# Kernel tuning notes

Hardware: AMD Instinct MI355X
Metric: run time of the kernel (lower is better)

## Reference

```python
import jax, jax.numpy as jnp
import numpy as np

B, S, E, H = 2, 2048, 1024, 16
HD = E // H  # 64
NEG = -1e24


def setup_inputs() -> dict:
    key = jax.random.key(0)
    ks = jax.random.split(key, 20)
    sc_e = 1.0 / np.sqrt(E)
    inp = {
        "q_matrix": jax.random.normal(ks[0], (B, S, E), jnp.float32),
        "k_matrix": jax.random.normal(ks[1], (B, S, E), jnp.float32),
        "v_matrix": jax.random.normal(ks[2], (B, S, E), jnp.float32),
        "mask": jax.random.randint(ks[3], (B, S, S), 0, 2).astype(bool),
        # global QKV projections (embed_dim -> embed_dim)
        "Wq": jax.random.normal(ks[4], (E, E), jnp.float32) * sc_e,
        "bq": jnp.zeros((E,), jnp.float32),
        "Wk": jax.random.normal(ks[5], (E, E), jnp.float32) * sc_e,
        "bk": jnp.zeros((E,), jnp.float32),
        "Wv": jax.random.normal(ks[6], (E, E), jnp.float32) * sc_e,
        "bv": jnp.zeros((E,), jnp.float32),
        # per-head QKV projections (embed_dim -> head_dim), batched over heads
        "Whq": jax.random.normal(ks[7], (H, E, HD), jnp.float32) * sc_e,
        "bhq": jnp.zeros((H, HD), jnp.float32),
        "Whk": jax.random.normal(ks[8], (H, E, HD), jnp.float32) * sc_e,
        "bhk": jnp.zeros((H, HD), jnp.float32),
        "Whv": jax.random.normal(ks[9], (H, E, HD), jnp.float32) * sc_e,
        "bhv": jnp.zeros((H, HD), jnp.float32),
        # output projection
        "Wo": jax.random.normal(ks[10], (E, E), jnp.float32) * sc_e,
        "bo": jnp.zeros((E,), jnp.float32),
    }
    return inp


def reference(q_matrix, k_matrix, v_matrix, mask, Wq, bq, Wk, bk, Wv, bv,
              Whq, bhq, Whk, bhk, Whv, bhv, Wo, bo):
    # global projections [B,S,E]
    qg = q_matrix @ Wq + bq
    kg = k_matrix @ Wk + bk
    vg = v_matrix @ Wv + bv
    # per-head projections -> [B,H,S,HD]
    qh = jnp.einsum('bse,hed->bhsd', qg, Whq) + bhq[None, :, None, :]
    kh = jnp.einsum('bse,hed->bhsd', kg, Whk) + bhk[None, :, None, :]
    vh = jnp.einsum('bse,hed->bhsd', vg, Whv) + bhv[None, :, None, :]
    # scaled dot-product attention, scores [B,H,S,S]
    scores = jnp.einsum('bhsd,bhtd->bhst', qh, kh) / jnp.sqrt(jnp.float32(HD))
    scores = jnp.where(mask[:, None, :, :], NEG, scores)
    weights = jax.nn.softmax(scores, axis=-1)
    out = jnp.einsum('bhst,bhtd->bhsd', weights, vh)
    # concat heads (head order along last dim, matching torch.cat)
    x = out.transpose(0, 2, 1, 3).reshape(out.shape[0], out.shape[2], E)
    return x @ Wo + bo
```

## Files before the change

### kernel.cpp

```cpp
#include <hip/hip_runtime.h>
#include <hip/hip_bf16.h>

typedef unsigned short us16;
typedef __attribute__((ext_vector_type(8))) short short8;
typedef __attribute__((ext_vector_type(4))) float float4v;

#define E_DIM 1024
#define S_LEN 2048
#define B_DIM 2
#define H_DIM 16
#define HD_DIM 64
#define M_ROWS 4096
#define SCALE2 0.18033688011112042f

__device__ __forceinline__ float b2f(us16 b) {
    return __uint_as_float(((unsigned int)b) << 16);
}
__device__ __forceinline__ us16 f2b(float f) {
    unsigned int u = __float_as_uint(f);
    unsigned int r = (u + 0x7fffu + ((u >> 16) & 1u)) >> 16;
    return (us16)r;
}

__device__ __forceinline__ void gload16(const us16* g, us16* lds_uniform_base) {
    __builtin_amdgcn_global_load_lds(
        (const __attribute__((address_space(1))) void*)g,
        (__attribute__((address_space(3))) void*)lds_uniform_base, 16, 0, 0);
}

__global__ __launch_bounds__(256) void prep(
    const float* __restrict__ q, const float* __restrict__ k, const float* __restrict__ v,
    const float* __restrict__ Wq, const float* __restrict__ Wk, const float* __restrict__ Wv,
    const float* __restrict__ Whq, const float* __restrict__ Whk, const float* __restrict__ Whv,
    const float* __restrict__ Wo,
    const float* __restrict__ bq, const float* __restrict__ bk, const float* __restrict__ bv,
    const float* __restrict__ bhq, const float* __restrict__ bhk, const float* __restrict__ bhv,
    const int* __restrict__ mask,
    us16* qb, us16* kb, us16* vb, us16* Wqb, us16* Wkb, us16* Wvb,
    us16* WhqT, us16* WhkT, us16* WhvT, us16* WoT,
    us16* marr,
    float* bcq, float* bck, float* bcv, float* zbias)
{
    __shared__ us16 tile[32][33];
    __shared__ float red[4][64];
    int blk = blockIdx.x, tid = threadIdx.x;

    if (blk < 7680) {
        const float* in; us16* out; int idx;
        if (blk < 6144) {
            int z = blk >> 11, rem = blk & 2047;
            in = z == 0 ? q : z == 1 ? k : v;
            out = z == 0 ? qb : z == 1 ? kb : vb;
            idx = (rem * 256 + tid) * 8;
        } else {
            int t = blk - 6144, z = t >> 9, rem = t & 511;
            in = z == 0 ? Wq : z == 1 ? Wk : Wv;
            out = z == 0 ? Wqb : z == 1 ? Wkb : Wvb;
            idx = (rem * 256 + tid) * 8;
        }
        float4 f0 = *(const float4*)(in + idx);
        float4 f1 = *(const float4*)(in + idx + 4);
        us16 t8[8] = {f2b(f0.x), f2b(f0.y), f2b(f0.z), f2b(f0.w),
                      f2b(f1.x), f2b(f1.y), f2b(f1.z), f2b(f1.w)};
        *(uint4*)(out + idx) = *(const uint4*)t8;
    } else if (blk < 11776) {
        int t = blk - 7680, z = t >> 10, rem = t & 1023;
        const float* in = z == 0 ? Whq : z == 1 ? Whk : z == 2 ? Whv : Wo;
        us16* out = z == 0 ? WhqT : z == 1 ? WhkT : z == 2 ? WhvT : WoT;
        int mode = (z < 3) ? 1 : 0;
        int bx = rem & 31, by = rem >> 5;
        int tx = tid & 31, ty = tid >> 5;
#pragma unroll
        for (int i = 0; i < 4; ++i) {
            int e = by * 32 + ty + i * 8;
            int c = bx * 32 + tx;
            size_t src;
            if (mode == 0) src = (size_t)e * E_DIM + c;
            else           src = ((size_t)(c >> 6) * E_DIM + e) * 64 + (c & 63);
            tile[ty + i * 8][tx] = f2b(in[src]);
        }
        __syncthreads();
#pragma unroll
        for (int i = 0; i < 4; ++i) {
            int c = bx * 32 + ty + i * 8;
            int e = by * 32 + tx;
            out[(size_t)c * E_DIM + e] = tile[tx][ty + i * 8];
        }
    } else if (blk < 15872) {
        int g = (blk - 11776) * 256 + tid;
        int lane = g & 63, ld = (g >> 6) & 1, wv = (g >> 7) & 7;
        int q0t = (g >> 10) & 15, ktz = (g >> 14) & 31, bb = g >> 19;
        int quad = lane >> 4, l16 = lane & 15;
        int qq = q0t * 128 + wv * 16 + l16;
        int t0 = ktz * 64 + ld * 32 + quad * 4;
        const int* mp = mask + ((size_t)bb * S_LEN + qq) * S_LEN + t0;
        int4 ma = *(const int4*)mp;
        int4 mb2 = *(const int4*)(mp + 16);
        const us16 NEGB = f2b(-1e38f);
        us16 t8[8];
        t8[0] = ma.x ? NEGB : (us16)0;  t8[1] = ma.y ? NEGB : (us16)0;
        t8[2] = ma.z ? NEGB : (us16)0;  t8[3] = ma.w ? NEGB : (us16)0;
        t8[4] = mb2.x ? NEGB : (us16)0; t8[5] = mb2.y ? NEGB : (us16)0;
        t8[6] = mb2.z ? NEGB : (us16)0; t8[7] = mb2.w ? NEGB : (us16)0;
        *(uint4*)&marr[(size_t)g * 8] = *(const uint4*)t8;
    } else if (blk < 15920) {
        int t = blk - 15872, z = t >> 4, h = t & 15;
        const float* bg = z == 0 ? bq : z == 1 ? bk : bv;
        const float* Wh = z == 0 ? Whq : z == 1 ? Whk : Whv;
        const float* bh = z == 0 ? bhq : z == 1 ? bhk : bhv;
        float* bc = z == 0 ? bcq : z == 1 ? bck : bcv;
        float sc = (z == 0) ? SCALE2 : 1.0f;
        int d = tid & 63, part = tid >> 6;
        float acc = 0.f;
        int j0 = part * 256;
        for (int j = j0; j < j0 + 256; ++j)
            acc += bg[j] * Wh[((size_t)h * E_DIM + j) * HD_DIM + d];
        red[part][d] = acc;
        __syncthreads();
        if (tid < 64)
            bc[h * 64 + tid] = (red[0][tid] + red[1][tid] + red[2][tid] + red[3][tid] + bh[h * 64 + tid]) * sc;
    } else {
        int i = (blk - 15920) * 256 + tid;
        if (i < 1024) zbias[i] = 0.f;
    }
}

#define BK 32

__device__ __forceinline__ void gemm_body(
    const us16* __restrict__ A, const us16* __restrict__ Bt,
    const float* __restrict__ bias, void* __restrict__ Cp,
    int M, int N, int K, int bxt, int byt, int omode)
{
    __shared__ us16 As[128 * BK];
    __shared__ us16 Bs[128 * BK];

    int tid = threadIdx.x;
    int wave = tid >> 6, lane = tid & 63;
    int quad = lane >> 4, l16 = lane & 15;
    int wm = (wave >> 1) * 64, wn = (wave & 1) * 64;
    int bm0 = byt * 128, bn0 = bxt * 128;
    int srow = lane >> 2;
    int gcol = (((lane & 3) ^ (srow & 3)) << 3);
    int rslot = ((quad ^ (l16 & 3)) << 3);

    float4v acc[4][4];
#pragma unroll
    for (int i = 0; i < 4; ++i)
#pragma unroll
        for (int j = 0; j < 4; ++j)
#pragma unroll
            for (int r = 0; r < 4; ++r) acc[i][j][r] = 0.f;

    for (int k0 = 0; k0 < K; k0 += BK) {
#pragma unroll
        for (int c = 0; c < 2; ++c) {
            int r0 = 32 * wave + 16 * c;
            gload16(A  + (size_t)(bm0 + r0 + srow) * K + k0 + gcol, &As[r0 * BK]);
            gload16(Bt + (size_t)(bn0 + r0 + srow) * K + k0 + gcol, &Bs[r0 * BK]);
        }
        __syncthreads();
        short8 af[4], bfr[4];
#pragma unroll
        for (int i = 0; i < 4; ++i)
            af[i] = *(const short8*)&As[(wm + i * 16 + l16) * BK + rslot];
#pragma unroll
        for (int j = 0; j < 4; ++j)
            bfr[j] = *(const short8*)&Bs[(wn + j * 16 + l16) * BK + rslot];
#pragma unroll
        for (int i = 0; i < 4; ++i)
#pragma unroll
            for (int j = 0; j < 4; ++j)
                acc[i][j] = __builtin_amdgcn_mfma_f32_16x16x32_bf16(af[i], bfr[j], acc[i][j], 0, 0, 0);
        __syncthreads();
    }

#pragma unroll
    for (int i = 0; i < 4; ++i) {
#pragma unroll
        for (int j = 0; j < 4; ++j) {
#pragma unroll
            for (int r = 0; r < 4; ++r) {
                int row = bm0 + wm + i * 16 + quad * 4 + r;
                int col = bn0 + wn + j * 16 + l16;
                float vv = acc[i][j][r] + ((omode == 3) ? bias[row] : bias[col]);
                if (omode == 1) {
                    int b = row >> 11, s = row & 2047, h = col >> 6, d = col & 63;
                    ((us16*)Cp)[(((size_t)(b * H_DIM + h) * S_LEN + s) * HD_DIM) + d] = f2b(vv);
                } else {
                    int h = row >> 6, d = row & 63, b = col >> 11, sl = col & 2047;
                    ((us16*)Cp)[(((size_t)(b * H_DIM + h) * HD_DIM + d) * S_LEN) + sl] = f2b(vv);
                }
            }
        }
    }
}

__global__ __launch_bounds__(256) void proj_all(
    const us16* __restrict__ qb, const us16* __restrict__ kb, const us16* __restrict__ vb,
    const us16* __restrict__ WcqT, const us16* __restrict__ WckT, const us16* __restrict__ WcvT,
    const float* __restrict__ bcq, const float* __restrict__ bck, const float* __restrict__ bcv,
    us16* __restrict__ qhb, us16* __restrict__ khb, us16* __restrict__ vtb)
{
    int bx = blockIdx.x;
    int z = bx >> 8, t = bx & 255;
    if (z == 0)      gemm_body(qb, WcqT, bcq, qhb, M_ROWS, E_DIM, E_DIM, t & 7, t >> 3, 1);
    else if (z == 1) gemm_body(kb, WckT, bck, khb, M_ROWS, E_DIM, E_DIM, t & 7, t >> 3, 1);
    else             gemm_body(WcvT, vb, bcv, vtb, E_DIM, M_ROWS, E_DIM, t & 31, t >> 5, 3);
}

template<int OMODE>
__device__ __forceinline__ void gemm64_body(
    const us16* __restrict__ A, const us16* __restrict__ Bt,
    const float* __restrict__ bias, void* __restrict__ Cp,
    int M, int N, int K, int bxt, int byt, float oscale)
{
    __shared__ us16 As[64 * BK];
    __shared__ us16 Bs[128 * BK];

    int tid = threadIdx.x;
    int wave = tid >> 6, lane = tid & 63;
    int quad = lane >> 4, l16 = lane & 15;
    int wm = (wave >> 1) * 32, wn = (wave & 1) * 64;
    int bm0 = byt * 64, bn0 = bxt * 128;
    int srow = lane >> 2;
    int gcol = (((lane & 3) ^ (srow & 3)) << 3);
    int rslot = ((quad ^ (l16 & 3)) << 3);

    float4v acc[2][4];
#pragma unroll
    for (int i = 0; i < 2; ++i)
#pragma unroll
        for (int j = 0; j < 4; ++j)
#pragma unroll
            for (int r = 0; r < 4; ++r) acc[i][j][r] = 0.f;

    for (int k0 = 0; k0 < K; k0 += BK) {
        gload16(A + (size_t)(bm0 + 16 * wave + srow) * K + k0 + gcol, &As[16 * wave * BK]);
#pragma unroll
        for (int c = 0; c < 2; ++c) {
            int r0 = 32 * wave + 16 * c;
            gload16(Bt + (size_t)(bn0 + r0 + srow) * K + k0 + gcol, &Bs[r0 * BK]);
        }
        __syncthreads();
        short8 af[2], bfr[4];
#pragma unroll
        for (int i = 0; i < 2; ++i)
            af[i] = *(const short8*)&As[(wm + i * 16 + l16) * BK + rslot];
#pragma unroll
        for (int j = 0; j < 4; ++j)
            bfr[j] = *(const short8*)&Bs[(wn + j * 16 + l16) * BK + rslot];
#pragma unroll
        for (int i = 0; i < 2; ++i)
#pragma unroll
            for (int j = 0; j < 4; ++j)
                acc[i][j] = __builtin_amdgcn_mfma_f32_16x16x32_bf16(af[i], bfr[j], acc[i][j], 0, 0, 0);
        __syncthreads();
    }

#pragma unroll
    for (int i = 0; i < 2; ++i)
#pragma unroll
        for (int j = 0; j < 4; ++j)
#pragma unroll
            for (int r = 0; r < 4; ++r) {
                int row = bm0 + wm + i * 16 + quad * 4 + r;
                int col = bn0 + wn + j * 16 + l16;
                float vv = (acc[i][j][r] + bias[col]) * oscale;
                if (OMODE == 0) ((us16*)Cp)[(size_t)row * N + col] = f2b(vv);
                else            ((float*)Cp)[(size_t)row * N + col] = vv;
            }
}

__global__ __launch_bounds__(256) void wgemm3(
    const us16* A0, const us16* A1, const us16* A2,
    const us16* B0, const us16* B1, const us16* B2,
    const float* zbias, us16* C0, us16* C1, us16* C2)
{
    int z = blockIdx.z;
    const us16* A = z == 0 ? A0 : z == 1 ? A1 : A2;
    const us16* Bt = z == 0 ? B0 : z == 1 ? B1 : B2;
    us16* C = z == 0 ? C0 : z == 1 ? C1 : C2;
    float sc = (z == 0) ? SCALE2 : 1.0f;
    gemm64_body<0>(A, Bt, zbias, C, E_DIM, E_DIM, E_DIM, blockIdx.x, blockIdx.y, sc);
}

__global__ __launch_bounds__(256) void gemm_out64(
    const us16* __restrict__ A, const us16* __restrict__ Bt,
    const float* __restrict__ bias, float* __restrict__ C, int M, int N, int K)
{
    gemm64_body<2>(A, Bt, bias, C, M, N, K, blockIdx.x, blockIdx.y, 1.0f);
}

#define PST 72
#define NT 16

__global__ __launch_bounds__(512) void attn_kernel(
    const us16* __restrict__ qh, const us16* __restrict__ kh,
    const us16* __restrict__ vt, const us16* __restrict__ marr,
    us16* __restrict__ o_p, float* __restrict__ l_p)
{
    __shared__ us16 Ks[2][64 * 64];
    __shared__ us16 Vs[2][64 * 64];
    __shared__ us16 Pw[8][16 * PST];

    int tid = threadIdx.x;
    int w = tid >> 6, lane = tid & 63;
    int quad = lane >> 4, l16 = lane & 15;

    int wg = blockIdx.x;
    int xcd = wg & 7, idx = wg >> 3;
    int bh = xcd * 4 + (idx >> 5);
    int rem = idx & 31;
    int z = rem >> 4;
    int q0t = rem & 15;
    int q0 = q0t * 128;
    int b = bh >> 4;
    const size_t base = (size_t)bh * (S_LEN * HD_DIM);

    int qrow = q0 + w * 16 + l16;
    short8 qf0, qf1;
    {
        const us16* qp = qh + base + (size_t)qrow * HD_DIM + quad * 8;
        qf0 = *(const short8*)qp;
        qf1 = *(const short8*)(qp + 32);
    }

    short8 onesf;
#pragma unroll
    for (int j = 0; j < 8; ++j) onesf[j] = (short)0x3F80;

    int strow = w * 8 + (lane >> 3);
    int scol = ((lane & 7) ^ (strow & 7)) * 8;
    const us16* ksrc0 = kh + base + ((size_t)(z * 1024 + strow)) * HD_DIM + scol;
    const us16* vsrc0 = vt + base + (size_t)strow * S_LEN + scol + z * 1024;

    const us16* mb0p = marr + ((((size_t)(b * 32 + z * 16) * 16 + q0t) * 8 + w) * 1024)
                            + (size_t)lane * 8;

    int slotA = (quad ^ (l16 & 7)) * 8;
    int slotB = slotA ^ 32;

    float4v o[4];
#pragma unroll
    for (int dt = 0; dt < 4; ++dt)
#pragma unroll
        for (int r = 0; r < 4; ++r) o[dt][r] = 0.f;
    float4v o_l;
#pragma unroll
    for (int r = 0; r < 4; ++r) o_l[r] = 0.f;

    auto QK = [&](const us16* KsC, uint4 m0, uint4 m1, float4v* sc) {
        __builtin_amdgcn_s_setprio(1);
#pragma unroll
        for (int ct = 0; ct < 4; ++ct) {
            int tt = ct * 16 + l16;
            short8 kf0 = *(const short8*)&KsC[tt * 64 + slotA];
            short8 kf1 = *(const short8*)&KsC[tt * 64 + slotB];
            unsigned w0, w1;
            if (ct == 0)      { w0 = m0.x; w1 = m0.y; }
            else if (ct == 1) { w0 = m0.z; w1 = m0.w; }
            else if (ct == 2) { w0 = m1.x; w1 = m1.y; }
            else              { w0 = m1.z; w1 = m1.w; }
            float4v a;
            a[0] = __uint_as_float(w0 << 16);
            a[1] = __uint_as_float(w0 & 0xFFFF0000u);
            a[2] = __uint_as_float(w1 << 16);
            a[3] = __uint_as_float(w1 & 0xFFFF0000u);
            a = __builtin_amdgcn_mfma_f32_16x16x32_bf16(kf0, qf0, a, 0, 0, 0);
            a = __builtin_amdgcn_mfma_f32_16x16x32_bf16(kf1, qf1, a, 0, 0, 0);
            sc[ct] = a;
        }
        __builtin_amdgcn_s_setprio(0);
    };

    gload16(ksrc0, &Ks[0][w * 512]);
    gload16(vsrc0, &Vs[0][w * 512]);
    gload16(ksrc0 + (size_t)64 * HD_DIM, &Ks[1][w * 512]);
    gload16(vsrc0 + 64, &Vs[1][w * 512]);
    uint4 mc0 = *(const uint4*)(mb0p);
    uint4 mc1 = *(const uint4*)(mb0p + 512);
    asm volatile("s_waitcnt vmcnt(2)" ::: "memory");
    __builtin_amdgcn_s_barrier();
    __builtin_amdgcn_sched_barrier(0);

    float4v sc[4];
    QK(Ks[0], mc0, mc1, sc);

    for (int t = 0; t < NT; ++t) {
        int cur = t & 1;

        uint4 mn0 = mc0, mn1 = mc1;
        if (t + 1 < NT) {
            const us16* mp = mb0p + (size_t)(t + 1) * 131072;
            mn0 = *(const uint4*)(mp);
            mn1 = *(const uint4*)(mp + 512);
        }

#pragma unroll
        for (int ct = 0; ct < 4; ++ct) {
            float p0 = __builtin_amdgcn_exp2f(sc[ct][0]);
            float p1 = __builtin_amdgcn_exp2f(sc[ct][1]);
            float p2 = __builtin_amdgcn_exp2f(sc[ct][2]);
            float p3 = __builtin_amdgcn_exp2f(sc[ct][3]);
            uint2 pk;
            asm("v_cvt_pk_bf16_f32 %0, %1, %2" : "=v"(pk.x) : "v"(p0), "v"(p1));
            asm("v_cvt_pk_bf16_f32 %0, %1, %2" : "=v"(pk.y) : "v"(p2), "v"(p3));
            *(uint2*)&Pw[w][l16 * PST + ct * 16 + quad * 4] = pk;
        }

        short8 pf0 = *(const short8*)&Pw[w][l16 * PST + quad * 8];
        short8 pf1 = *(const short8*)&Pw[w][l16 * PST + 32 + quad * 8];
        const us16* VsC = Vs[cur];
        __builtin_amdgcn_s_setprio(1);
#pragma unroll
        for (int dt = 0; dt < 4; ++dt) {
            int d = dt * 16 + l16;
            short8 vf0 = *(const short8*)&VsC[d * 64 + slotA];
            short8 vf1 = *(const short8*)&VsC[d * 64 + slotB];
            o[dt] = __builtin_amdgcn_mfma_f32_16x16x32_bf16(pf0, vf0, o[dt], 0, 0, 0);
            o[dt] = __builtin_amdgcn_mfma_f32_16x16x32_bf16(pf1, vf1, o[dt], 0, 0, 0);
        }
        o_l = __builtin_amdgcn_mfma_f32_16x16x32_bf16(pf0, onesf, o_l, 0, 0, 0);
        o_l = __builtin_amdgcn_mfma_f32_16x16x32_bf16(pf1, onesf, o_l, 0, 0, 0);
        __builtin_amdgcn_s_setprio(0);

        if (t + 1 == NT) break;

        __builtin_amdgcn_s_barrier();
        __builtin_amdgcn_sched_barrier(0);

        if (t + 2 < NT) {
            gload16(ksrc0 + (size_t)((t + 2) * 64) * HD_DIM, &Ks[cur][w * 512]);
            gload16(vsrc0 + (t + 2) * 64, &Vs[cur][w * 512]);
            asm volatile("s_waitcnt vmcnt(2)" ::: "memory");
        } else {
            asm volatile("s_waitcnt vmcnt(0)" ::: "memory");
        }
        __builtin_amdgcn_s_barrier();
        __builtin_amdgcn_sched_barrier(0);

        mc0 = mn0; mc1 = mn1;
        QK(Ks[cur ^ 1], mc0, mc1, sc);
    }

    if (l16 == 0) {
#pragma unroll
        for (int r = 0; r < 4; ++r)
            l_p[(size_t)z * 65536 + bh * S_LEN + q0 + w * 16 + quad * 4 + r] = o_l[r];
    }

    int rowg = bh * S_LEN + q0 + w * 16 + quad * 4;
#pragma unroll
    for (int dt = 0; dt < 4; ++dt)
#pragma unroll
        for (int r = 0; r < 4; ++r)
            o_p[(size_t)z * 4194304 + (size_t)(rowg + r) * 64 + dt * 16 + l16] = f2b(o[dt][r]);
}

__global__ __launch_bounds__(256) void attn_combine(
    const us16* __restrict__ o_p, const float* __restrict__ l_p,
    us16* __restrict__ x)
{
    int fidx = blockIdx.x * 256 + threadIdx.x;
    int rix = fidx >> 3;
    int d8 = (fidx & 7) * 8;
    float linv = 1.0f / (l_p[rix] + l_p[65536 + rix]);
    uint4 a = *(const uint4*)(o_p + (size_t)rix * 64 + d8);
    uint4 c = *(const uint4*)(o_p + 4194304 + (size_t)rix * 64 + d8);
    const us16* ap = (const us16*)&a;
    const us16* cp = (const us16*)&c;
    us16 t8[8];
#pragma unroll
    for (int i = 0; i < 8; ++i)
        t8[i] = f2b((b2f(ap[i]) + b2f(cp[i])) * linv);
    int bh = rix >> 11, b = bh >> 4, h = bh & 15, s = rix & 2047;
    *(uint4*)&x[(size_t)(b * S_LEN + s) * E_DIM + h * HD_DIM + d8] = *(const uint4*)t8;
}

extern "C" void kernel_launch(void* const* d_in, const int* in_sizes, int n_in,
                              void* d_out, int out_size, void* d_ws, size_t ws_size,
                              hipStream_t stream) {
    const float* q    = (const float*)d_in[0];
    const float* k    = (const float*)d_in[1];
    const float* v    = (const float*)d_in[2];
    const int*   mask = (const int*)d_in[3];
    const float* Wq = (const float*)d_in[4];   const float* bq = (const float*)d_in[5];
    const float* Wk = (const float*)d_in[6];   const float* bk = (const float*)d_in[7];
    const float* Wv = (const float*)d_in[8];   const float* bv = (const float*)d_in[9];
    const float* Whq = (const float*)d_in[10]; const float* bhq = (const float*)d_in[11];
    const float* Whk = (const float*)d_in[12]; const float* bhk = (const float*)d_in[13];
    const float* Whv = (const float*)d_in[14]; const float* bhv = (const float*)d_in[15];
    const float* Wo = (const float*)d_in[16];  const float* bo = (const float*)d_in[17];

    us16* ws = (us16*)d_ws;
    const size_t M1 = (size_t)1 << 20;
    us16* WhqT = ws + 0 * M1;
    us16* WhkT = ws + 1 * M1;
    us16* WhvT = ws + 2 * M1;
    us16* WoT  = ws + 3 * M1;
    us16* WcqT = ws + 4 * M1;
    us16* WckT = ws + 5 * M1;
    us16* WcvT = ws + 6 * M1;
    us16* Wqb  = ws + 7 * M1;
    us16* Wkb  = ws + 8 * M1;
    us16* Wvb  = ws + 9 * M1;
    us16* qb   = ws + 10 * M1;
    us16* kb   = ws + 14 * M1;
    us16* vb   = ws + 18 * M1;
    us16* qhb  = ws + 22 * M1;
    us16* khb  = ws + 26 * M1;
    us16* vtb  = ws + 30 * M1;
    us16* o_p  = qb;
    us16* xb   = vb;
    float* bcq   = (float*)(ws + 34 * M1);
    float* bck   = bcq + 1024;
    float* bcv   = bck + 1024;
    float* zbias = bcv + 1024;
    float* l_p   = (float*)(ws + 34 * M1 + 8192);
    us16*  marr  = ws + 35 * M1;

    prep<<<15924, 256, 0, stream>>>(q, k, v, Wq, Wk, Wv, Whq, Whk, Whv, Wo,
                                    bq, bk, bv, bhq, bhk, bhv, mask,
                                    qb, kb, vb, Wqb, Wkb, Wvb,
                                    WhqT, WhkT, WhvT, WoT, marr,
                                    bcq, bck, bcv, zbias);

    wgemm3<<<dim3(8, 16, 3), 256, 0, stream>>>(WhqT, WhkT, WhvT, Wqb, Wkb, Wvb, zbias,
                                               WcqT, WckT, WcvT);

    proj_all<<<768, 256, 0, stream>>>(qb, kb, vb, WcqT, WckT, WcvT,
                                      bcq, bck, bcv, qhb, khb, vtb);

    attn_kernel<<<1024, 512, 0, stream>>>(qhb, khb, vtb, marr, o_p, l_p);
    attn_combine<<<2048, 256, 0, stream>>>(o_p, l_p, xb);

    gemm_out64<<<dim3(8, 64), 256, 0, stream>>>(xb, WoT, bo, (float*)d_out,
                                                M_ROWS, E_DIM, E_DIM);
}
```

Before: 304.6 us.

## Drop split-KV attention and fuse normalization into the attention kernel

Result: faster. 298.3 us (-2.1%).

```diff
diff --git a/kernel.cpp b/kernel.cpp
--- a/kernel.cpp
+++ b/kernel.cpp
@@ -293,12 +293,12 @@
 }
 
 #define PST 72
-#define NT 16
+#define NT 32
 
 __global__ __launch_bounds__(512) void attn_kernel(
     const us16* __restrict__ qh, const us16* __restrict__ kh,
     const us16* __restrict__ vt, const us16* __restrict__ marr,
-    us16* __restrict__ o_p, float* __restrict__ l_p)
+    us16* __restrict__ x)
 {
     __shared__ us16 Ks[2][64 * 64];
     __shared__ us16 Vs[2][64 * 64];
@@ -310,10 +310,8 @@
 
     int wg = blockIdx.x;
     int xcd = wg & 7, idx = wg >> 3;
-    int bh = xcd * 4 + (idx >> 5);
-    int rem = idx & 31;
-    int z = rem >> 4;
-    int q0t = rem & 15;
+    int bh = xcd * 4 + (idx >> 4);
+    int q0t = idx & 15;
     int q0 = q0t * 128;
     int b = bh >> 4;
     const size_t base = (size_t)bh * (S_LEN * HD_DIM);
@@ -332,10 +330,10 @@
 
     int strow = w * 8 + (lane >> 3);
     int scol = ((lane & 7) ^ (strow & 7)) * 8;
-    const us16* ksrc0 = kh + base + ((size_t)(z * 1024 + strow)) * HD_DIM + scol;
-    const us16* vsrc0 = vt + base + (size_t)strow * S_LEN + scol + z * 1024;
-
-    const us16* mb0p = marr + ((((size_t)(b * 32 + z * 16) * 16 + q0t) * 8 + w) * 1024)
+    const us16* ksrc0 = kh + base + (size_t)strow * HD_DIM + scol;
+    const us16* vsrc0 = vt + base + (size_t)strow * S_LEN + scol;
+
+    const us16* mb0p = marr + ((((size_t)(b * 32) * 16 + q0t) * 8 + w) * 1024)
                             + (size_t)lane * 8;
 
     int slotA = (quad ^ (l16 & 7)) * 8;
@@ -444,38 +442,18 @@
         QK(Ks[cur ^ 1], mc0, mc1, sc);
     }
 
-    if (l16 == 0) {
-#pragma unroll
-        for (int r = 0; r < 4; ++r)
-            l_p[(size_t)z * 65536 + bh * S_LEN + q0 + w * 16 + quad * 4 + r] = o_l[r];
-    }
-
-    int rowg = bh * S_LEN + q0 + w * 16 + quad * 4;
-#pragma unroll
-    for (int dt = 0; dt < 4; ++dt)
-#pragma unroll
-        for (int r = 0; r < 4; ++r)
-            o_p[(size_t)z * 4194304 + (size_t)(rowg + r) * 64 + dt * 16 + l16] = f2b(o[dt][r]);
-}
-
-__global__ __launch_bounds__(256) void attn_combine(
-    const us16* __restrict__ o_p, const float* __restrict__ l_p,
-    us16* __restrict__ x)
-{
-    int fidx = blockIdx.x * 256 + threadIdx.x;
-    int rix = fidx >> 3;
-    int d8 = (fidx & 7) * 8;
-    float linv = 1.0f / (l_p[rix] + l_p[65536 + rix]);
-    uint4 a = *(const uint4*)(o_p + (size_t)rix * 64 + d8);
-    uint4 c = *(const uint4*)(o_p + 4194304 + (size_t)rix * 64 + d8);
-    const us16* ap = (const us16*)&a;
-    const us16* cp = (const us16*)&c;
-    us16 t8[8];
-#pragma unroll
-    for (int i = 0; i < 8; ++i)
-        t8[i] = f2b((b2f(ap[i]) + b2f(cp[i])) * linv);
-    int bh = rix >> 11, b = bh >> 4, h = bh & 15, s = rix & 2047;
-    *(uint4*)&x[(size_t)(b * S_LEN + s) * E_DIM + h * HD_DIM + d8] = *(const uint4*)t8;
+    float linv[4];
+#pragma unroll
+    for (int r = 0; r < 4; ++r) linv[r] = 1.0f / o_l[r];
+    int h = bh & 15;
+    int srow0 = q0 + w * 16 + quad * 4;
+#pragma unroll
+    for (int r = 0; r < 4; ++r) {
+        size_t xro = ((size_t)(b * S_LEN + srow0 + r)) * E_DIM + h * HD_DIM;
+#pragma unroll
+        for (int dt = 0; dt < 4; ++dt)
+            x[xro + dt * 16 + l16] = f2b(o[dt][r] * linv[r]);
+    }
 }
 
 extern "C" void kernel_launch(void* const* d_in, const int* in_sizes, int n_in,
@@ -511,13 +489,11 @@
     us16* qhb  = ws + 22 * M1;
     us16* khb  = ws + 26 * M1;
     us16* vtb  = ws + 30 * M1;
-    us16* o_p  = qb;
     us16* xb   = vb;
     float* bcq   = (float*)(ws + 34 * M1);
     float* bck   = bcq + 1024;
     float* bcv   = bck + 1024;
     float* zbias = bcv + 1024;
-    float* l_p   = (float*)(ws + 34 * M1 + 8192);
     us16*  marr  = ws + 35 * M1;
 
     prep<<<15924, 256, 0, stream>>>(q, k, v, Wq, Wk, Wv, Whq, Whk, Whv, Wo,
@@ -532,8 +508,7 @@
     proj_all<<<768, 256, 0, stream>>>(qb, kb, vb, WcqT, WckT, WcvT,
                                       bcq, bck, bcv, qhb, khb, vtb);
 
-    attn_kernel<<<1024, 512, 0, stream>>>(qhb, khb, vtb, marr, o_p, l_p);
-    attn_combine<<<2048, 256, 0, stream>>>(o_p, l_p, xb);
+    attn_kernel<<<512, 512, 0, stream>>>(qhb, khb, vtb, marr, xb);
 
     gemm_out64<<<dim3(8, 64), 256, 0, stream>>>(xb, WoT, bo, (float*)d_out,
                                                 M_ROWS, E_DIM, E_DIM);
```
